# Performance work log

Measured on AMD Instinct MI355X. Metric: run time of the kernel, lower is better.

## Reference

```python
import jax, jax.numpy as jnp
import numpy as np

EMBED = 1024
HEADS = 16
HEAD_DIM = EMBED // HEADS
SCALING = HEAD_DIM ** -0.5
R = 16
LORA_SCALE = 32.0 / R  # alpha / r
NEG = jnp.finfo(jnp.float32).min


def lora_linear(x, W, A, B):
    # y = x @ W.T + (x @ A.T) @ B.T * scale   (LinearLora, bias=False)
    return x @ W.T + ((x @ A.T) @ B.T) * LORA_SCALE


def setup_inputs() -> dict:
    key = jax.random.key(0)
    ks = jax.random.split(key, 14)
    B, T, D = 1, 4096, EMBED
    hidden_states = jax.random.normal(ks[0], (B, T, D), jnp.float32)
    # causal additive mask (bsz, 1, tgt, src): 0 on/below diag, dtype-min above
    i = jnp.arange(T)
    causal = jnp.where(i[:, None] >= i[None, :], 0.0, NEG).astype(jnp.float32)
    attention_mask = jnp.broadcast_to(causal, (B, 1, T, T))
    s = 0.02
    def w(k, shape):
        return jax.random.normal(k, shape, jnp.float32) * s
    return dict(
        hidden_states=hidden_states,
        attention_mask=attention_mask,
        Wq=w(ks[1], (D, D)), Wk=w(ks[2], (D, D)), Wv=w(ks[3], (D, D)), Wo=w(ks[4], (D, D)),
        Aq=w(ks[5], (R, D)), Bq=jnp.zeros((D, R), jnp.float32) + w(ks[6], (D, R)),
        Ak=w(ks[7], (R, D)), Bk=w(ks[8], (D, R)),
        Av=w(ks[9], (R, D)), Bv=w(ks[10], (D, R)),
        Ao=w(ks[11], (R, D)), Bo=w(ks[12], (D, R)),
    )


def reference(hidden_states, attention_mask, Wq, Wk, Wv, Wo,
              Aq, Bq, Ak, Bk, Av, Bv, Ao, Bo):
    bsz, tgt_len, _ = hidden_states.shape
    H, Hd = HEADS, HEAD_DIM

    q = lora_linear(hidden_states, Wq, Aq, Bq) * SCALING
    k = lora_linear(hidden_states, Wk, Ak, Bk)
    v = lora_linear(hidden_states, Wv, Av, Bv)

    # (b, t, H, Hd)
    q = q.reshape(bsz, tgt_len, H, Hd)
    k = k.reshape(bsz, tgt_len, H, Hd)
    v = v.reshape(bsz, tgt_len, H, Hd)

    # scores (b, H, t, s)
    attn = jnp.einsum('bthd,bshd->bhts', q, k)
    attn = attn + attention_mask
    attn = jnp.maximum(attn, NEG)
    attn = jax.nn.softmax(attn, axis=-1)  # dropout p=0 / eval mode

    out = jnp.einsum('bhts,bshd->bthd', attn, v)
    out = out.reshape(bsz, tgt_len, H * Hd)
    out = lora_linear(out, Wo, Ao, Bo)
    return out
```

## Files before the change

### kernel.cpp

```cpp
#include <hip/hip_runtime.h>
#include <cmath>
#include <cstdint>

typedef unsigned short u16;
typedef __attribute__((ext_vector_type(8))) __bf16 bf16x8;
typedef __attribute__((ext_vector_type(4))) __bf16 bf16x4;
typedef __attribute__((ext_vector_type(4))) short s16x4;
typedef __attribute__((ext_vector_type(4))) float f32x4;

__device__ __forceinline__ u16 f2bf(float f) {
    union { float f; unsigned u; } v; v.f = f;
    unsigned r = v.u + 0x7fffu + ((v.u >> 16) & 1u);
    return (u16)(r >> 16);
}

__device__ __forceinline__ void gload_lds(const u16* g, u16* l) {
    __builtin_amdgcn_global_load_lds((__attribute__((address_space(1))) void*)g,
                                     (__attribute__((address_space(3))) void*)l,
                                     16, 0, 0);
}

__device__ __forceinline__ f32x4 mfma16(s16x4 a, s16x4 b, f32x4 c) {
#if __has_builtin(__builtin_amdgcn_mfma_f32_16x16x16bf16_1k)
    return __builtin_amdgcn_mfma_f32_16x16x16bf16_1k(a, b, c, 0, 0, 0);
#else
    asm("v_mfma_f32_16x16x16_bf16 %0, %1, %2, %3"
        : "=v"(c) : "v"(a), "v"(b), "0"(c));
    return c;
#endif
}


__global__ __launch_bounds__(256) void x_to_bf16(const float4* __restrict__ X,
                                                 ushort4* __restrict__ Xb) {
    int i = blockIdx.x * 256 + threadIdx.x;
    float4 v = X[i];
    ushort4 o;
    o.x = f2bf(v.x); o.y = f2bf(v.y); o.z = f2bf(v.z); o.w = f2bf(v.w);
    Xb[i] = o;
}

__global__ __launch_bounds__(256) void prep_weff(
        const float* __restrict__ Wq, const float* __restrict__ Wk,
        const float* __restrict__ Wv, const float* __restrict__ Wo,
        const float* __restrict__ Aq, const float* __restrict__ Bq,
        const float* __restrict__ Ak, const float* __restrict__ Bk,
        const float* __restrict__ Av, const float* __restrict__ Bv,
        const float* __restrict__ Ao, const float* __restrict__ Bo,
        u16* __restrict__ Wqkv, u16* __restrict__ Wob) {
    const int p = blockIdx.y;
    const int idx = blockIdx.x * 256 + threadIdx.x;
    const int n = idx >> 10, d = idx & 1023;
    const float* W; const float* A; const float* B;
    switch (p) {
        case 0: W = Wq; A = Aq; B = Bq; break;
        case 1: W = Wk; A = Ak; B = Bk; break;
        case 2: W = Wv; A = Av; B = Bv; break;
        default: W = Wo; A = Ao; B = Bo; break;
    }
    float lora = 0.f;
#pragma unroll
    for (int r = 0; r < 16; r++) lora += B[n * 16 + r] * A[r * 1024 + d];
    float v = W[idx] + 2.0f * lora;
    if (p == 0) v *= 0.125f * 1.44269504088896340736f;
    if (p < 3) Wqkv[(size_t)p * 1048576 + idx] = f2bf(v);
    else       Wob[idx] = f2bf(v);
}

template <bool F32OUT>
__global__ __launch_bounds__(256) void gemm_bt(const u16* __restrict__ A,
                                               const u16* __restrict__ B,
                                               void* __restrict__ C, int ldc) {
    __shared__ __align__(16) u16 As[128 * 32];
    __shared__ __align__(16) u16 Bs[128 * 32];
    const int tid = threadIdx.x;
    const int lane = tid & 63, wave = tid >> 6;
    const int quad = lane >> 4, l16 = lane & 15;
    const int wm = (wave >> 1) * 64, wn = (wave & 1) * 64;
    const size_t m0 = (size_t)blockIdx.y * 128, n0 = (size_t)blockIdx.x * 128;
    const u16* Ap = A + m0 * 1024;
    const u16* Bp = B + n0 * 1024;
    f32x4 acc[4][4] = {};
    for (int k0 = 0; k0 < 1024; k0 += 32) {
#pragma unroll
        for (int hh = 0; hh < 2; hh++) {
            int c = tid + hh * 256;
            int row = c >> 2, cp = (c & 3) * 8;
            gload_lds(Ap + (size_t)row * 1024 + k0 + cp, As + c * 8);
            gload_lds(Bp + (size_t)row * 1024 + k0 + cp, Bs + c * 8);
        }
        __syncthreads();
        bf16x8 af[4], bfr[4];
#pragma unroll
        for (int i = 0; i < 4; i++) {
            af[i]  = *(const bf16x8*)(As + (wm + i * 16 + l16) * 32 + quad * 8);
            bfr[i] = *(const bf16x8*)(Bs + (wn + i * 16 + l16) * 32 + quad * 8);
        }
#pragma unroll
        for (int mi = 0; mi < 4; mi++)
#pragma unroll
            for (int ni = 0; ni < 4; ni++)
                acc[mi][ni] = __builtin_amdgcn_mfma_f32_16x16x32_bf16(
                        af[mi], bfr[ni], acc[mi][ni], 0, 0, 0);
        __syncthreads();
    }
#pragma unroll
    for (int mi = 0; mi < 4; mi++)
#pragma unroll
        for (int ni = 0; ni < 4; ni++)
#pragma unroll
            for (int r = 0; r < 4; r++) {
                size_t row = m0 + wm + mi * 16 + quad * 4 + r;
                size_t col = n0 + wn + ni * 16 + l16;
                if (F32OUT) ((float*)C)[row * ldc + col] = acc[mi][ni][r];
                else        ((u16*)C)[row * ldc + col] = f2bf(acc[mi][ni][r]);
            }
}

__global__ __launch_bounds__(256) void transpose_v(const u16* __restrict__ Y,
                                                   u16* __restrict__ Vt) {
    __shared__ u16 tile[64][68];
    const int dv0 = blockIdx.x * 64;
    const int t0  = blockIdx.y * 64;
    const int tid = threadIdx.x;
#pragma unroll
    for (int p = 0; p < 4; p++) {
        int pos = tid + p * 256;
        int row = pos >> 4;
        int c4  = (pos & 15) * 4;
        ushort4 v = *(const ushort4*)(Y + (size_t)(t0 + row) * 3072 + 2048 + dv0 + c4);
        tile[row][c4 + 0] = v.x; tile[row][c4 + 1] = v.y;
        tile[row][c4 + 2] = v.z; tile[row][c4 + 3] = v.w;
    }
    __syncthreads();
#pragma unroll
    for (int p = 0; p < 4; p++) {
        int pos = tid + p * 256;
        int orow = pos >> 4;
        int oc4  = (pos & 15) * 4;
        ushort4 o;
        o.x = tile[oc4 + 0][orow]; o.y = tile[oc4 + 1][orow];
        o.z = tile[oc4 + 2][orow]; o.w = tile[oc4 + 3][orow];
        *(ushort4*)(Vt + (size_t)(dv0 + orow) * 4096 + t0 + oc4) = o;
    }
}

__global__ __launch_bounds__(256, 4) void flash_attn(const u16* __restrict__ Y,
                                                     const u16* __restrict__ Vt,
                                                     u16* __restrict__ O) {
    __shared__ __align__(16) u16 lds[16384];
    const int tid = threadIdx.x;
    const int wave = tid >> 6, lane = tid & 63;
    const int quad = lane >> 4, l16 = lane & 15;
    const int bid = blockIdx.x;
    const int rr = bid & 255, j = bid >> 8;
    const int b = rr >> 4, h = rr & 15;
    int p;
    switch (j) { case 0:  p = 63 - b; break;
                 case 1:  p = 32 + b; break;
                 case 2:  p = 31 - b; break;
                 default: p = b;      break; }
    const int q0 = p * 64;
    const int q0w = q0 + wave * 16;
    const int nT = p + 1;
    const u16* Kbase = Y + 1024 + h * 64;
    const u16* Vbase = Vt + (size_t)(h * 64) * 4096;
    const int xsw = l16 & 7;

    bf16x8 qf[2];
#pragma unroll
    for (int kf = 0; kf < 2; kf++)
        qf[kf] = *(const bf16x8*)(Y + (size_t)(q0w + l16) * 3072
                                    + h * 64 + kf * 32 + quad * 8);

    f32x4 oaccT[4] = {};
    float l_i = 0.f;

#pragma unroll
    for (int pp = 0; pp < 2; pp++) {
        int c = pp * 256 + tid;
        int row = c >> 3, cg = (c & 7) ^ (row & 7);
        gload_lds(Kbase + (size_t)row * 3072 + cg * 8, lds + c * 8);
        gload_lds(Vbase + (size_t)row * 4096 + cg * 8, lds + 4096 + c * 8);
    }

#pragma unroll 1
    for (int t = 0; t < nT; t++) {
        const int s0 = t * 64;
        u16* Ks = lds + (t & 1) * 8192;
        u16* Vs = Ks + 4096;
        asm volatile("s_waitcnt vmcnt(0)" ::: "memory");
        __syncthreads();

        if (t + 1 < nT) {
            u16* Kn = lds + ((t + 1) & 1) * 8192;
            const int sn = s0 + 64;
#pragma unroll
            for (int pp = 0; pp < 2; pp++) {
                int c = pp * 256 + tid;
                int row = c >> 3, cg = (c & 7) ^ (row & 7);
                gload_lds(Kbase + (size_t)(sn + row) * 3072 + cg * 8, Kn + c * 8);
                gload_lds(Vbase + (size_t)row * 4096 + sn + cg * 8, Kn + 4096 + c * 8);
            }
        }

        bf16x8 kfr[4][2];
#pragma unroll
        for (int ni = 0; ni < 4; ni++) {
            int row = ni * 16 + l16;
            kfr[ni][0] = *(const bf16x8*)(Ks + row * 64 + ((quad) ^ xsw) * 8);
            kfr[ni][1] = *(const bf16x8*)(Ks + row * 64 + ((4 + quad) ^ xsw) * 8);
        }
        s16x4 vfr[4][4];
#pragma unroll
        for (int nj = 0; nj < 4; nj++) {
            int row = nj * 16 + l16;
#pragma unroll
            for (int ni = 0; ni < 4; ni++) {
                int cc = ni * 2 + (quad >> 1);
                vfr[nj][ni] = *(const s16x4*)(Vs + row * 64 + (cc ^ xsw) * 8
                                                 + (quad & 1) * 4);
            }
        }
        asm volatile("s_waitcnt lgkmcnt(0)" ::: "memory");

        f32x4 sacc[4] = {};
#pragma unroll
        for (int ni = 0; ni < 4; ni++) {
            sacc[ni] = __builtin_amdgcn_mfma_f32_16x16x32_bf16(
                    kfr[ni][0], qf[0], sacc[ni], 0, 0, 0);
            sacc[ni] = __builtin_amdgcn_mfma_f32_16x16x32_bf16(
                    kfr[ni][1], qf[1], sacc[ni], 0, 0, 0);
        }

        if (t == nT - 1) {
            const int qg = q0w + l16;
#pragma unroll
            for (int ni = 0; ni < 4; ni++)
#pragma unroll
                for (int r = 0; r < 4; r++) {
                    int sg = s0 + ni * 16 + quad * 4 + r;
                    if (sg > qg) sacc[ni][r] = -INFINITY;
                }
        }
        float rs = 0.f;
        s16x4 pf[4];
#pragma unroll
        for (int ni = 0; ni < 4; ni++) {
            f32x4 pe;
#pragma unroll
            for (int r = 0; r < 4; r++) {
                pe[r] = __builtin_amdgcn_exp2f(sacc[ni][r]);
                rs += pe[r];
            }
            bf16x4 tt = { (__bf16)pe[0], (__bf16)pe[1],
                          (__bf16)pe[2], (__bf16)pe[3] };
            pf[ni] = __builtin_bit_cast(s16x4, tt);
        }
        rs += __shfl_xor(rs, 16);
        rs += __shfl_xor(rs, 32);
        l_i += rs;

#pragma unroll
        for (int nj = 0; nj < 4; nj++)
#pragma unroll
            for (int ni = 0; ni < 4; ni++)
                oaccT[nj] = mfma16(vfr[nj][ni], pf[ni], oaccT[nj]);
    }

    __syncthreads();
    u16* scr = lds + wave * 1152;
    {
        float inv = 1.0f / l_i;
#pragma unroll
        for (int nj = 0; nj < 4; nj++) {
            bf16x4 t4 = { (__bf16)(oaccT[nj][0] * inv),
                          (__bf16)(oaccT[nj][1] * inv),
                          (__bf16)(oaccT[nj][2] * inv),
                          (__bf16)(oaccT[nj][3] * inv) };
            *(s16x4*)(scr + l16 * 72 + nj * 16 + quad * 4) =
                    __builtin_bit_cast(s16x4, t4);
        }
    }
    asm volatile("s_waitcnt lgkmcnt(0)" ::: "memory");
#pragma unroll
    for (int pp = 0; pp < 2; pp++) {
        int row = pp * 8 + (lane >> 3);
        int seg = (lane & 7) * 8;
        bf16x8 d = *(const bf16x8*)(scr + row * 72 + seg);
        *(bf16x8*)(O + (size_t)(q0w + row) * 1024 + h * 64 + seg) = d;
    }
}


extern "C" void kernel_launch(void* const* d_in, const int* in_sizes, int n_in,
                              void* d_out, int out_size, void* d_ws, size_t ws_size,
                              hipStream_t stream) {
    const float* X  = (const float*)d_in[0];
    const float* Wq = (const float*)d_in[2];
    const float* Wk = (const float*)d_in[3];
    const float* Wv = (const float*)d_in[4];
    const float* Wo = (const float*)d_in[5];
    const float* Aq = (const float*)d_in[6];
    const float* Bq = (const float*)d_in[7];
    const float* Ak = (const float*)d_in[8];
    const float* Bk = (const float*)d_in[9];
    const float* Av = (const float*)d_in[10];
    const float* Bv = (const float*)d_in[11];
    const float* Ao = (const float*)d_in[12];
    const float* Bo = (const float*)d_in[13];

    char* ws = (char*)d_ws;
    u16* Xb   = (u16*)(ws);
    u16* Wqkv = (u16*)(ws + (8u  << 20));
    u16* Wob  = (u16*)(ws + (14u << 20));
    u16* Y    = (u16*)(ws + (16u << 20));
    u16* Vt   = (u16*)(ws + (40u << 20));
    u16* Ob   = (u16*)(ws + (48u << 20));

    x_to_bf16<<<4096, 256, 0, stream>>>((const float4*)X, (ushort4*)Xb);
    prep_weff<<<dim3(4096, 4), 256, 0, stream>>>(Wq, Wk, Wv, Wo, Aq, Bq, Ak, Bk,
                                                 Av, Bv, Ao, Bo, Wqkv, Wob);
    gemm_bt<false><<<dim3(24, 32), 256, 0, stream>>>(Xb, Wqkv, Y, 3072);
    transpose_v<<<dim3(16, 64), 256, 0, stream>>>(Y, Vt);
    flash_attn<<<dim3(1024), 256, 0, stream>>>(Y, Vt, Ob);
    gemm_bt<true><<<dim3(8, 32), 256, 0, stream>>>(Ob, Wob, d_out, 1024);
}
```

Before: 271.8 us.

## Pair causal tiles per block, fuse prep kernels, add smaller-tile output GEMM

Merges the X conversion and weight-prep kernels into a single launch. Flash attention now runs 512 blocks, and each block handles two query tiles (p and 63-p) in sequence so every block does the same amount of causal work. It also drops the occupancy hint and moves the V fragment loads after the QK MFMAs. The output projection uses a new 64x128-tile GEMM so more blocks share the GPU, at the cost of less data reuse per block and a non-pipelined K loop.

```diff
diff --git a/kernel.cpp b/kernel.cpp
--- a/kernel.cpp
+++ b/kernel.cpp
@@ -30,26 +30,24 @@
 #endif
 }
 
-
-__global__ __launch_bounds__(256) void x_to_bf16(const float4* __restrict__ X,
-                                                 ushort4* __restrict__ Xb) {
-    int i = blockIdx.x * 256 + threadIdx.x;
-    float4 v = X[i];
-    ushort4 o;
-    o.x = f2bf(v.x); o.y = f2bf(v.y); o.z = f2bf(v.z); o.w = f2bf(v.w);
-    Xb[i] = o;
-}
-
-__global__ __launch_bounds__(256) void prep_weff(
+__global__ __launch_bounds__(256) void prep_all(
+        const float* __restrict__ X,
         const float* __restrict__ Wq, const float* __restrict__ Wk,
         const float* __restrict__ Wv, const float* __restrict__ Wo,
         const float* __restrict__ Aq, const float* __restrict__ Bq,
         const float* __restrict__ Ak, const float* __restrict__ Bk,
         const float* __restrict__ Av, const float* __restrict__ Bv,
         const float* __restrict__ Ao, const float* __restrict__ Bo,
-        u16* __restrict__ Wqkv, u16* __restrict__ Wob) {
+        u16* __restrict__ Wqkv, u16* __restrict__ Wob, u16* __restrict__ Xb) {
     const int p = blockIdx.y;
     const int idx = blockIdx.x * 256 + threadIdx.x;
+    if (p == 4) {
+        float4 v = ((const float4*)X)[idx];
+        ushort4 o;
+        o.x = f2bf(v.x); o.y = f2bf(v.y); o.z = f2bf(v.z); o.w = f2bf(v.w);
+        ((ushort4*)Xb)[idx] = o;
+        return;
+    }
     const int n = idx >> 10, d = idx & 1023;
     const float* W; const float* A; const float* B;
     switch (p) {
@@ -117,6 +115,61 @@
             }
 }
 
+template <bool F32OUT>
+__global__ __launch_bounds__(256) void gemm_bt64(const u16* __restrict__ A,
+                                                 const u16* __restrict__ B,
+                                                 void* __restrict__ C, int ldc) {
+    __shared__ __align__(16) u16 As[64 * 32];
+    __shared__ __align__(16) u16 Bs[128 * 32];
+    const int tid = threadIdx.x;
+    const int lane = tid & 63, wave = tid >> 6;
+    const int quad = lane >> 4, l16 = lane & 15;
+    const int wm = (wave >> 1) * 32, wn = (wave & 1) * 64;
+    const size_t m0 = (size_t)blockIdx.y * 64, n0 = (size_t)blockIdx.x * 128;
+    const u16* Ap = A + m0 * 1024;
+    const u16* Bp = B + n0 * 1024;
+    f32x4 acc[2][4] = {};
+    for (int k0 = 0; k0 < 1024; k0 += 32) {
+        {
+            int c = tid;
+            int row = c >> 2, cp = (c & 3) * 8;
+            gload_lds(Ap + (size_t)row * 1024 + k0 + cp, As + c * 8);
+#pragma unroll
+            for (int hh = 0; hh < 2; hh++) {
+                int b = hh * 256 + tid;
+                int brow = b >> 2, bcp = (b & 3) * 8;
+                gload_lds(Bp + (size_t)brow * 1024 + k0 + bcp, Bs + b * 8);
+            }
+        }
+        __syncthreads();
+        bf16x8 af[2], bfr[4];
+#pragma unroll
+        for (int i = 0; i < 2; i++)
+            af[i] = *(const bf16x8*)(As + (wm + i * 16 + l16) * 32 + quad * 8);
+#pragma unroll
+        for (int i = 0; i < 4; i++)
+            bfr[i] = *(const bf16x8*)(Bs + (wn + i * 16 + l16) * 32 + quad * 8);
+#pragma unroll
+        for (int mi = 0; mi < 2; mi++)
+#pragma unroll
+            for (int ni = 0; ni < 4; ni++)
+                acc[mi][ni] = __builtin_amdgcn_mfma_f32_16x16x32_bf16(
+                        af[mi], bfr[ni], acc[mi][ni], 0, 0, 0);
+        __syncthreads();
+    }
+#pragma unroll
+    for (int mi = 0; mi < 2; mi++)
+#pragma unroll
+        for (int ni = 0; ni < 4; ni++)
+#pragma unroll
+            for (int r = 0; r < 4; r++) {
+                size_t row = m0 + wm + mi * 16 + quad * 4 + r;
+                size_t col = n0 + wn + ni * 16 + l16;
+                if (F32OUT) ((float*)C)[row * ldc + col] = acc[mi][ni][r];
+                else        ((u16*)C)[row * ldc + col] = f2bf(acc[mi][ni][r]);
+            }
+}
+
 __global__ __launch_bounds__(256) void transpose_v(const u16* __restrict__ Y,
                                                    u16* __restrict__ Vt) {
     __shared__ u16 tile[64][68];
@@ -145,150 +198,148 @@
     }
 }
 
-__global__ __launch_bounds__(256, 4) void flash_attn(const u16* __restrict__ Y,
-                                                     const u16* __restrict__ Vt,
-                                                     u16* __restrict__ O) {
+__global__ __launch_bounds__(256) void flash_attn(const u16* __restrict__ Y,
+                                                  const u16* __restrict__ Vt,
+                                                  u16* __restrict__ O) {
     __shared__ __align__(16) u16 lds[16384];
     const int tid = threadIdx.x;
     const int wave = tid >> 6, lane = tid & 63;
     const int quad = lane >> 4, l16 = lane & 15;
-    const int bid = blockIdx.x;
-    const int rr = bid & 255, j = bid >> 8;
-    const int b = rr >> 4, h = rr & 15;
-    int p;
-    switch (j) { case 0:  p = 63 - b; break;
-                 case 1:  p = 32 + b; break;
-                 case 2:  p = 31 - b; break;
-                 default: p = b;      break; }
-    const int q0 = p * 64;
-    const int q0w = q0 + wave * 16;
-    const int nT = p + 1;
+    const int h = blockIdx.x & 15;
+    const int pr = blockIdx.x >> 4;
     const u16* Kbase = Y + 1024 + h * 64;
     const u16* Vbase = Vt + (size_t)(h * 64) * 4096;
     const int xsw = l16 & 7;
 
-    bf16x8 qf[2];
-#pragma unroll
-    for (int kf = 0; kf < 2; kf++)
-        qf[kf] = *(const bf16x8*)(Y + (size_t)(q0w + l16) * 3072
-                                    + h * 64 + kf * 32 + quad * 8);
-
-    f32x4 oaccT[4] = {};
-    float l_i = 0.f;
-
-#pragma unroll
-    for (int pp = 0; pp < 2; pp++) {
-        int c = pp * 256 + tid;
-        int row = c >> 3, cg = (c & 7) ^ (row & 7);
-        gload_lds(Kbase + (size_t)row * 3072 + cg * 8, lds + c * 8);
-        gload_lds(Vbase + (size_t)row * 4096 + cg * 8, lds + 4096 + c * 8);
-    }
-
 #pragma unroll 1
-    for (int t = 0; t < nT; t++) {
-        const int s0 = t * 64;
-        u16* Ks = lds + (t & 1) * 8192;
-        u16* Vs = Ks + 4096;
-        asm volatile("s_waitcnt vmcnt(0)" ::: "memory");
-        __syncthreads();
-
-        if (t + 1 < nT) {
-            u16* Kn = lds + ((t + 1) & 1) * 8192;
-            const int sn = s0 + 64;
-#pragma unroll
-            for (int pp = 0; pp < 2; pp++) {
-                int c = pp * 256 + tid;
-                int row = c >> 3, cg = (c & 7) ^ (row & 7);
-                gload_lds(Kbase + (size_t)(sn + row) * 3072 + cg * 8, Kn + c * 8);
-                gload_lds(Vbase + (size_t)row * 4096 + sn + cg * 8, Kn + 4096 + c * 8);
-            }
-        }
-
-        bf16x8 kfr[4][2];
-#pragma unroll
-        for (int ni = 0; ni < 4; ni++) {
-            int row = ni * 16 + l16;
-            kfr[ni][0] = *(const bf16x8*)(Ks + row * 64 + ((quad) ^ xsw) * 8);
-            kfr[ni][1] = *(const bf16x8*)(Ks + row * 64 + ((4 + quad) ^ xsw) * 8);
-        }
-        s16x4 vfr[4][4];
-#pragma unroll
-        for (int nj = 0; nj < 4; nj++) {
-            int row = nj * 16 + l16;
+    for (int ph = 0; ph < 2; ph++) {
+        const int p = ph ? (63 - pr) : pr;
+        const int q0w = p * 64 + wave * 16;
+        const int nT = p + 1;
+
+        bf16x8 qf[2];
+#pragma unroll
+        for (int kf = 0; kf < 2; kf++)
+            qf[kf] = *(const bf16x8*)(Y + (size_t)(q0w + l16) * 3072
+                                        + h * 64 + kf * 32 + quad * 8);
+
+        f32x4 oaccT[4] = {};
+        float l_i = 0.f;
+
+#pragma unroll
+        for (int pp = 0; pp < 2; pp++) {
+            int c = pp * 256 + tid;
+            int row = c >> 3, cg = (c & 7) ^ (row & 7);
+            gload_lds(Kbase + (size_t)row * 3072 + cg * 8, lds + c * 8);
+            gload_lds(Vbase + (size_t)row * 4096 + cg * 8, lds + 4096 + c * 8);
+        }
+
+#pragma unroll 1
+        for (int t = 0; t < nT; t++) {
+            const int s0 = t * 64;
+            u16* Ks = lds + (t & 1) * 8192;
+            u16* Vs = Ks + 4096;
+            asm volatile("s_waitcnt vmcnt(0)" ::: "memory");
+            __syncthreads();
+
+            if (t + 1 < nT) {
+                u16* Kn = lds + ((t + 1) & 1) * 8192;
+                const int sn = s0 + 64;
+#pragma unroll
+                for (int pp = 0; pp < 2; pp++) {
+                    int c = pp * 256 + tid;
+                    int row = c >> 3, cg = (c & 7) ^ (row & 7);
+                    gload_lds(Kbase + (size_t)(sn + row) * 3072 + cg * 8, Kn + c * 8);
+                    gload_lds(Vbase + (size_t)row * 4096 + sn + cg * 8, Kn + 4096 + c * 8);
+                }
+            }
+
+            bf16x8 kfr[4][2];
 #pragma unroll
             for (int ni = 0; ni < 4; ni++) {
-                int cc = ni * 2 + (quad >> 1);
-                vfr[nj][ni] = *(const s16x4*)(Vs + row * 64 + (cc ^ xsw) * 8
-                                                 + (quad & 1) * 4);
+                int row = ni * 16 + l16;
+                kfr[ni][0] = *(const bf16x8*)(Ks + row * 64 + ((quad) ^ xsw) * 8);
+                kfr[ni][1] = *(const bf16x8*)(Ks + row * 64 + ((4 + quad) ^ xsw) * 8);
+            }
+            f32x4 sacc[4] = {};
+#pragma unroll
+            for (int ni = 0; ni < 4; ni++) {
+                sacc[ni] = __builtin_amdgcn_mfma_f32_16x16x32_bf16(
+                        kfr[ni][0], qf[0], sacc[ni], 0, 0, 0);
+                sacc[ni] = __builtin_amdgcn_mfma_f32_16x16x32_bf16(
+                        kfr[ni][1], qf[1], sacc[ni], 0, 0, 0);
+            }
+            s16x4 vfr[4][4];
+#pragma unroll
+            for (int nj = 0; nj < 4; nj++) {
+                int row = nj * 16 + l16;
+#pragma unroll
+                for (int ni = 0; ni < 4; ni++) {
+                    int cc = ni * 2 + (quad >> 1);
+                    vfr[nj][ni] = *(const s16x4*)(Vs + row * 64 + (cc ^ xsw) * 8
+                                                     + (quad & 1) * 4);
+                }
+            }
+
+            if (t == nT - 1) {
+                const int qg = q0w + l16;
+#pragma unroll
+                for (int ni = 0; ni < 4; ni++)
+#pragma unroll
+                    for (int r = 0; r < 4; r++) {
+                        int sg = s0 + ni * 16 + quad * 4 + r;
+                        if (sg > qg) sacc[ni][r] = -INFINITY;
+                    }
+            }
+            float rs = 0.f;
+            s16x4 pf[4];
+#pragma unroll
+            for (int ni = 0; ni < 4; ni++) {
+                f32x4 pe;
+#pragma unroll
+                for (int r = 0; r < 4; r++) {
+                    pe[r] = __builtin_amdgcn_exp2f(sacc[ni][r]);
+                    rs += pe[r];
+                }
+                bf16x4 tt = { (__bf16)pe[0], (__bf16)pe[1],
+                              (__bf16)pe[2], (__bf16)pe[3] };
+                pf[ni] = __builtin_bit_cast(s16x4, tt);
+            }
+            rs += __shfl_xor(rs, 16);
+            rs += __shfl_xor(rs, 32);
+            l_i += rs;
+
+#pragma unroll
+            for (int nj = 0; nj < 4; nj++)
+#pragma unroll
+                for (int ni = 0; ni < 4; ni++)
+                    oaccT[nj] = mfma16(vfr[nj][ni], pf[ni], oaccT[nj]);
+        }
+
+        __syncthreads();
+        u16* scr = lds + wave * 1152;
+        {
+            float inv = 1.0f / l_i;
+#pragma unroll
+            for (int nj = 0; nj < 4; nj++) {
+                bf16x4 t4 = { (__bf16)(oaccT[nj][0] * inv),
+                              (__bf16)(oaccT[nj][1] * inv),
+                              (__bf16)(oaccT[nj][2] * inv),
+                              (__bf16)(oaccT[nj][3] * inv) };
+                *(s16x4*)(scr + l16 * 72 + nj * 16 + quad * 4) =
+                        __builtin_bit_cast(s16x4, t4);
             }
         }
         asm volatile("s_waitcnt lgkmcnt(0)" ::: "memory");
-
-        f32x4 sacc[4] = {};
-#pragma unroll
-        for (int ni = 0; ni < 4; ni++) {
-            sacc[ni] = __builtin_amdgcn_mfma_f32_16x16x32_bf16(
-                    kfr[ni][0], qf[0], sacc[ni], 0, 0, 0);
-            sacc[ni] = __builtin_amdgcn_mfma_f32_16x16x32_bf16(
-                    kfr[ni][1], qf[1], sacc[ni], 0, 0, 0);
-        }
-
-        if (t == nT - 1) {
-            const int qg = q0w + l16;
-#pragma unroll
-            for (int ni = 0; ni < 4; ni++)
-#pragma unroll
-                for (int r = 0; r < 4; r++) {
-                    int sg = s0 + ni * 16 + quad * 4 + r;
-                    if (sg > qg) sacc[ni][r] = -INFINITY;
-                }
-        }
-        float rs = 0.f;
-        s16x4 pf[4];
-#pragma unroll
-        for (int ni = 0; ni < 4; ni++) {
-            f32x4 pe;
-#pragma unroll
-            for (int r = 0; r < 4; r++) {
-                pe[r] = __builtin_amdgcn_exp2f(sacc[ni][r]);
-                rs += pe[r];
-            }
-            bf16x4 tt = { (__bf16)pe[0], (__bf16)pe[1],
-                          (__bf16)pe[2], (__bf16)pe[3] };
-            pf[ni] = __builtin_bit_cast(s16x4, tt);
-        }
-        rs += __shfl_xor(rs, 16);
-        rs += __shfl_xor(rs, 32);
-        l_i += rs;
-
-#pragma unroll
-        for (int nj = 0; nj < 4; nj++)
-#pragma unroll
-            for (int ni = 0; ni < 4; ni++)
-                oaccT[nj] = mfma16(vfr[nj][ni], pf[ni], oaccT[nj]);
-    }
-
-    __syncthreads();
-    u16* scr = lds + wave * 1152;
-    {
-        float inv = 1.0f / l_i;
-#pragma unroll
-        for (int nj = 0; nj < 4; nj++) {
-            bf16x4 t4 = { (__bf16)(oaccT[nj][0] * inv),
-                          (__bf16)(oaccT[nj][1] * inv),
-                          (__bf16)(oaccT[nj][2] * inv),
-                          (__bf16)(oaccT[nj][3] * inv) };
-            *(s16x4*)(scr + l16 * 72 + nj * 16 + quad * 4) =
-                    __builtin_bit_cast(s16x4, t4);
-        }
-    }
-    asm volatile("s_waitcnt lgkmcnt(0)" ::: "memory");
-#pragma unroll
-    for (int pp = 0; pp < 2; pp++) {
-        int row = pp * 8 + (lane >> 3);
-        int seg = (lane & 7) * 8;
-        bf16x8 d = *(const bf16x8*)(scr + row * 72 + seg);
-        *(bf16x8*)(O + (size_t)(q0w + row) * 1024 + h * 64 + seg) = d;
+#pragma unroll
+        for (int pp = 0; pp < 2; pp++) {
+            int row = pp * 8 + (lane >> 3);
+            int seg = (lane & 7) * 8;
+            bf16x8 d = *(const bf16x8*)(scr + row * 72 + seg);
+            *(bf16x8*)(O + (size_t)(p * 64 + wave * 16 + row) * 1024
+                         + h * 64 + seg) = d;
+        }
+        __syncthreads();
     }
 }
 
@@ -318,11 +369,10 @@
     u16* Vt   = (u16*)(ws + (40u << 20));
     u16* Ob   = (u16*)(ws + (48u << 20));
 
-    x_to_bf16<<<4096, 256, 0, stream>>>((const float4*)X, (ushort4*)Xb);
-    prep_weff<<<dim3(4096, 4), 256, 0, stream>>>(Wq, Wk, Wv, Wo, Aq, Bq, Ak, Bk,
-                                                 Av, Bv, Ao, Bo, Wqkv, Wob);
+    prep_all<<<dim3(4096, 5), 256, 0, stream>>>(X, Wq, Wk, Wv, Wo, Aq, Bq, Ak, Bk,
+                                                Av, Bv, Ao, Bo, Wqkv, Wob, Xb);
     gemm_bt<false><<<dim3(24, 32), 256, 0, stream>>>(Xb, Wqkv, Y, 3072);
     transpose_v<<<dim3(16, 64), 256, 0, stream>>>(Y, Vt);
-    flash_attn<<<dim3(1024), 256, 0, stream>>>(Y, Vt, Ob);
-    gemm_bt<true><<<dim3(8, 32), 256, 0, stream>>>(Ob, Wob, d_out, 1024);
-}
+    flash_attn<<<dim3(512), 256, 0, stream>>>(Y, Vt, Ob);
+    gemm_bt64<true><<<dim3(8, 64), 256, 0, stream>>>(Ob, Wob, d_out, 1024);
+}
```

Result: slower. 279.7 us (+2.9%).
